# Optimization experiments

Measured on AMD Instinct MI355X. Metric: run time of the kernel, lower is better.

The kernel has to match this reference:

```python
import jax, jax.numpy as jnp
import numpy as np

N_NODES = 100000
N_EDGES = 1000000
N_GRAPHS = 2048
IN_DIM, HIDDEN, OUT_DIM = 5, 64, 128


def setup_inputs() -> dict:
    key = jax.random.key(0)
    ks = jax.random.split(key, 12)
    x = jax.random.normal(ks[0], (N_NODES, IN_DIM), dtype=jnp.float32)
    edge_index = jax.random.randint(ks[1], (2, N_EDGES), 0, N_NODES, dtype=jnp.int64)
    batch = jnp.sort(jax.random.randint(ks[2], (N_NODES,), 0, N_GRAPHS, dtype=jnp.int64))
    def lin(k, fan_in, fan_out):
        bound = 1.0 / np.sqrt(fan_in)
        kw, kb = jax.random.split(k)
        W = jax.random.uniform(kw, (fan_in, fan_out), jnp.float32, -bound, bound)
        b = jax.random.uniform(kb, (fan_out,), jnp.float32, -bound, bound)
        return W, b
    W1, b1 = lin(ks[3], IN_DIM, HIDDEN)
    W2, b2 = lin(ks[4], HIDDEN, HIDDEN)
    W3, b3 = lin(ks[5], HIDDEN, HIDDEN)
    W4, b4 = lin(ks[6], HIDDEN, OUT_DIM)
    return {"x": x, "edge_index": edge_index, "batch": batch,
            "W1": W1, "b1": b1, "W2": W2, "b2": b2,
            "W3": W3, "b3": b3, "W4": W4, "b4": b4}


def _gcn_conv(x, W, b, src, dst, norm, n):
    # h = x W; message from src, scaled by symmetric norm, scattered to dst
    h = x @ W                                   # [N, F]
    msg = h[src] * norm[:, None]                # [E+N, F] gather
    agg = jax.ops.segment_sum(msg, dst, num_segments=n)  # scatter-add
    return agg + b


def reference(x, edge_index, batch, W1, b1, W2, b2, W3, b3, W4, b4):
    n = x.shape[0]
    loop = jnp.arange(n, dtype=edge_index.dtype)
    # GCN with self-loops: src -> dst aggregation, D^-1/2 A_hat D^-1/2 norm
    src = jnp.concatenate([edge_index[0], loop])
    dst = jnp.concatenate([edge_index[1], loop])
    deg = jax.ops.segment_sum(jnp.ones_like(dst, dtype=x.dtype), dst, num_segments=n)
    dinv = jnp.where(deg > 0, jax.lax.rsqrt(jnp.maximum(deg, 1.0)), 0.0)
    norm = dinv[src] * dinv[dst]                # [E+N]

    h = jax.nn.relu(_gcn_conv(x, W1, b1, src, dst, norm, n))
    h = jax.nn.relu(_gcn_conv(h, W2, b2, src, dst, norm, n))

    # global mean pool per graph
    sums = jax.ops.segment_sum(h, batch, num_segments=N_GRAPHS)      # [G, F]
    cnts = jax.ops.segment_sum(jnp.ones((n,), h.dtype), batch, num_segments=N_GRAPHS)
    pooled = sums / jnp.maximum(cnts, 1.0)[:, None]

    # MLP head
    z = jax.nn.relu(pooled @ W3 + b3)
    return z @ W4 + b4
```

## Files before the change

### kernel.cpp

```cpp
#include <hip/hip_runtime.h>
#include <hip/hip_fp16.h>

#define N_NODES  100000
#define N_EDGES  1000000
#define N_GRAPHS 2048
#define IN_DIM   5
#define HIDDEN   64
#define OUT_DIM  128
#define CAP      32
#define NA       512
#define PART     256
#define NBIN     391
#define LSTR     72

typedef _Float16 f16x8 __attribute__((ext_vector_type(8)));
typedef float    f32x4 __attribute__((ext_vector_type(4)));

__global__ void k_hist(const int* __restrict__ dst, int* __restrict__ histT) {
    __shared__ int h[NBIN];
    int t = threadIdx.x, b = blockIdx.x;
    for (int i = t; i < NBIN; i += 256) h[i] = 0;
    __syncthreads();
    for (int e = b * 256 + t; e < N_EDGES; e += NA * 256)
        atomicAdd(&h[dst[e] >> 8], 1);
    __syncthreads();
    for (int i = t; i < NBIN; i += 256) histT[i * NA + b] = h[i];
}

__global__ void k_scanA(int* __restrict__ histT, int* __restrict__ total) {
    __shared__ int s[2][256];
    int bin = blockIdx.x, t = threadIdx.x;
    int* col = histT + bin * NA;
    int v0 = col[2 * t], v1 = col[2 * t + 1];
    int pair = v0 + v1;
    int cur = 0;
    s[0][t] = pair;
    __syncthreads();
    for (int off = 1; off < 256; off <<= 1) {
        int nv = s[cur][t] + ((t >= off) ? s[cur][t - off] : 0);
        s[cur ^ 1][t] = nv;
        cur ^= 1;
        __syncthreads();
    }
    int incl = s[cur][t];
    int excl = incl - pair;
    col[2 * t]     = excl;
    col[2 * t + 1] = excl + v0;
    if (t == 255) total[bin] = incl;
}

__global__ void k_scanB(const int* __restrict__ total, int* __restrict__ binBase) {
    __shared__ int s[2][512];
    int t = threadIdx.x;
    int v = (t < NBIN) ? total[t] : 0;
    int cur = 0;
    s[0][t] = v;
    __syncthreads();
    for (int off = 1; off < 512; off <<= 1) {
        int nv = s[cur][t] + ((t >= off) ? s[cur][t - off] : 0);
        s[cur ^ 1][t] = nv;
        cur ^= 1;
        __syncthreads();
    }
    if (t < NBIN) binBase[t] = s[cur][t] - v;
    if (t == NBIN - 1) binBase[NBIN] = s[cur][t];
}

__global__ void k_part(const int* __restrict__ src, const int* __restrict__ dst,
                       const int* __restrict__ histT, const int* __restrict__ binBase,
                       int* __restrict__ epart) {
    __shared__ int off[NBIN];
    int t = threadIdx.x, b = blockIdx.x;
    for (int i = t; i < NBIN; i += 256)
        off[i] = binBase[i] + histT[i * NA + b];
    __syncthreads();
    for (int e = b * 256 + t; e < N_EDGES; e += NA * 256) {
        int d = dst[e];
        int pos = atomicAdd(&off[d >> 8], 1);
        epart[pos] = ((d & (PART - 1)) << 17) | src[e];
    }
}

__global__ void __launch_bounds__(256) k_build(
        const int* __restrict__ epart, const int* __restrict__ binBase,
        const float* __restrict__ x, int* __restrict__ cnt, int* __restrict__ bkt,
        float* __restrict__ dinv, __half* __restrict__ xs) {
    __shared__ int lcnt[PART];
    __shared__ int lrows[PART * CAP];
    int t = threadIdx.x, b = blockIdx.x;
    int base = b * PART;
    for (int i = t; i < PART; i += 256) lcnt[i] = 0;
    __syncthreads();
    int estart = binBase[b], eend = binBase[b + 1];
    for (int i = estart + t; i < eend; i += 256) {
        int ed = epart[i];
        int ln = ed >> 17;
        int c = atomicAdd(&lcnt[ln], 1);
        if (c < CAP) lrows[ln * CAP + c] = ed & 0x1FFFF;
    }
    __syncthreads();
    int gbase = base * CAP;
    int lim = min(PART * CAP, N_NODES * CAP - gbase);
    for (int i = t; i < lim; i += 256) bkt[gbase + i] = lrows[i];
    for (int n = t; n < PART; n += 256) {
        int g = base + n;
        if (g < N_NODES) {
            int c = lcnt[n];
            cnt[g] = c;
            float d = rsqrtf(1.0f + (float)c);
            dinv[g] = d;
#pragma unroll
            for (int k = 0; k < 8; k++)
                xs[(size_t)g * 8 + k] =
                    __float2half((k < IN_DIM) ? x[g * IN_DIM + k] * d : 0.0f);
        }
    }
}

__global__ void __launch_bounds__(256) k_g5l12(
        const int* __restrict__ cnt, const int* __restrict__ bkt,
        const __half* __restrict__ xs,
        const float* __restrict__ W1, const float* __restrict__ b1,
        const float* __restrict__ W2, const float* __restrict__ dinv,
        __half* __restrict__ hs2h) {
    __shared__ _Float16 lh1[64 * LSTR];
    __shared__ _Float16 lw2[64 * LSTR];
    __shared__ float la5[64][8];
    int tid = threadIdx.x;
    int w = tid >> 6, l = tid & 63;
    int nodeBase = blockIdx.x * 64;

#pragma unroll
    for (int i = 0; i < 16; i++) {
        int idx = tid + i * 256;
        int k = idx >> 6, n = idx & 63;
        lw2[n * LSTR + k] = (_Float16)W2[k * HIDDEN + n];
    }

    {
        int g4 = l >> 2, l4 = l & 3;
        int ln = w * 16 + g4;
        int g = nodeBase + ln;
        float accx = 0.f, accy = 0.f;
        if (g < N_NODES) {
            const __half2* XH = (const __half2*)xs;
            int len = min(cnt[g], CAP);
            const int* row = bkt + (size_t)g * CAP;
            float2 self = __half22float2(XH[(size_t)g * 4 + l4]);
            accx = self.x; accy = self.y;
            for (int e = 0; e < len; e++) {
                int s = row[e];
                float2 v = __half22float2(XH[(size_t)s * 4 + l4]);
                accx += v.x; accy += v.y;
            }
            float d = dinv[g];
            accx *= d; accy *= d;
        }
        la5[ln][l4 * 2]     = accx;
        la5[ln][l4 * 2 + 1] = accy;
    }

    int f = l;
    for (int i = 0; i < 16; i++) {
        int ln = w * 16 + i;
        float t1 = b1[f];
#pragma unroll
        for (int k = 0; k < IN_DIM; k++)
            t1 += la5[ln][k] * W1[k * HIDDEN + f];
        lh1[ln * LSTR + f] = (_Float16)fmaxf(t1, 0.f);
    }
    __syncthreads();

    int quad = l >> 4, m16 = l & 15;
    f32x4 acc0 = {0.f, 0.f, 0.f, 0.f};
    f32x4 acc1 = {0.f, 0.f, 0.f, 0.f};
    f32x4 acc2 = {0.f, 0.f, 0.f, 0.f};
    f32x4 acc3 = {0.f, 0.f, 0.f, 0.f};
#pragma unroll
    for (int kc = 0; kc < 2; kc++) {
        f16x8 a = *(const f16x8*)&lh1[(w * 16 + m16) * LSTR + kc * 32 + quad * 8];
        f16x8 b0 = *(const f16x8*)&lw2[(0 * 16 + m16) * LSTR + kc * 32 + quad * 8];
        f16x8 b1f = *(const f16x8*)&lw2[(1 * 16 + m16) * LSTR + kc * 32 + quad * 8];
        f16x8 b2 = *(const f16x8*)&lw2[(2 * 16 + m16) * LSTR + kc * 32 + quad * 8];
        f16x8 b3 = *(const f16x8*)&lw2[(3 * 16 + m16) * LSTR + kc * 32 + quad * 8];
        acc0 = __builtin_amdgcn_mfma_f32_16x16x32_f16(a, b0, acc0, 0, 0, 0);
        acc1 = __builtin_amdgcn_mfma_f32_16x16x32_f16(a, b1f, acc1, 0, 0, 0);
        acc2 = __builtin_amdgcn_mfma_f32_16x16x32_f16(a, b2, acc2, 0, 0, 0);
        acc3 = __builtin_amdgcn_mfma_f32_16x16x32_f16(a, b3, acc3, 0, 0, 0);
    }
#pragma unroll
    for (int i = 0; i < 4; i++) {
        int g = nodeBase + w * 16 + quad * 4 + i;
        if (g >= N_NODES) continue;
        float dv = dinv[g];
        __half* row = hs2h + (size_t)g * HIDDEN + m16;
        row[0]  = __float2half(acc0[i] * dv);
        row[16] = __float2half(acc1[i] * dv);
        row[32] = __float2half(acc2[i] * dv);
        row[48] = __float2half(acc3[i] * dv);
    }
}

__global__ void k_gather2(const int* __restrict__ cnt, const int* __restrict__ bkt,
                          const __half* __restrict__ hs2h,
                          const float* __restrict__ dinv,
                          float* __restrict__ agg2) {
    int tid = threadIdx.x;
    int w = tid >> 6, lane = tid & 63;
    int g16 = lane >> 4, l16 = lane & 15;
    int node = blockIdx.x * 16 + w * 4 + g16;
    if (node >= N_NODES) return;
    int len = min(cnt[node], CAP);
    const int* row = bkt + (size_t)node * CAP;
    const float2* H8 = (const float2*)hs2h;
    float ax = 0.f, ay = 0.f, az = 0.f, aw = 0.f;
    float bx = 0.f, by = 0.f, bz = 0.f, bw = 0.f;
    int idx = 0;
    for (; idx + 1 < len; idx += 2) {
        int s0 = row[idx], s1 = row[idx + 1];
        float2 r0 = H8[(size_t)s0 * 16 + l16];
        float2 r1 = H8[(size_t)s1 * 16 + l16];
        const __half2* h0 = (const __half2*)&r0;
        const __half2* h1 = (const __half2*)&r1;
        float2 u0 = __half22float2(h0[0]), u1 = __half22float2(h0[1]);
        float2 v0 = __half22float2(h1[0]), v1 = __half22float2(h1[1]);
        ax += u0.x; ay += u0.y; az += u1.x; aw += u1.y;
        bx += v0.x; by += v0.y; bz += v1.x; bw += v1.y;
    }
    if (idx < len) {
        int s0 = row[idx];
        float2 r0 = H8[(size_t)s0 * 16 + l16];
        const __half2* h0 = (const __half2*)&r0;
        float2 u0 = __half22float2(h0[0]), u1 = __half22float2(h0[1]);
        ax += u0.x; ay += u0.y; az += u1.x; aw += u1.y;
    }
    float2 rs = H8[(size_t)node * 16 + l16];
    const __half2* hs = (const __half2*)&rs;
    float2 s0 = __half22float2(hs[0]), s1 = __half22float2(hs[1]);
    float d = dinv[node];
    float4 o;
    o.x = (ax + bx + s0.x) * d;
    o.y = (ay + by + s0.y) * d;
    o.z = (az + bz + s1.x) * d;
    o.w = (aw + bw + s1.y) * d;
    ((float4*)agg2)[(size_t)node * 16 + l16] = o;
}

__global__ void k_head(const float* __restrict__ agg2, const float* __restrict__ b2,
                       const int* __restrict__ batch,
                       const float* __restrict__ W3, const float* __restrict__ b3,
                       const float* __restrict__ W4, const float* __restrict__ b4,
                       float* __restrict__ out) {
    __shared__ int range[2];
    __shared__ float part[2][HIDDEN];
    __shared__ float p[HIDDEN];
    __shared__ float z[HIDDEN];
    int g = blockIdx.x, tid = threadIdx.x;
    if (tid < 2) {
        int v = g + tid;
        int lo = 0, hi = N_NODES;
        while (lo < hi) {
            int m = (lo + hi) >> 1;
            if (batch[m] < v) lo = m + 1; else hi = m;
        }
        range[tid] = lo;
    }
    __syncthreads();
    int s = range[0], e = range[1];
    int f = tid & 63, half = tid >> 6;
    float acc = 0.f;
    float bb = b2[f];
    for (int node = s + half; node < e; node += 2)
        acc += fmaxf(agg2[(size_t)node * HIDDEN + f] + bb, 0.f);
    part[half][f] = acc;
    __syncthreads();
    if (tid < HIDDEN) {
        float inv = 1.0f / fmaxf((float)(e - s), 1.0f);
        p[tid] = (part[0][tid] + part[1][tid]) * inv;
    }
    __syncthreads();
    if (tid < HIDDEN) {
        float t = b3[tid];
#pragma unroll 8
        for (int k = 0; k < HIDDEN; k++) t += p[k] * W3[k * HIDDEN + tid];
        z[tid] = fmaxf(t, 0.f);
    }
    __syncthreads();
    float t = b4[tid];
#pragma unroll 8
    for (int k = 0; k < HIDDEN; k++) t += z[k] * W4[k * OUT_DIM + tid];
    out[(size_t)g * OUT_DIM + tid] = t;
}

extern "C" void kernel_launch(void* const* d_in, const int* in_sizes, int n_in,
                              void* d_out, int out_size, void* d_ws, size_t ws_size,
                              hipStream_t stream) {
    const float* x  = (const float*)d_in[0];
    const int*   ei = (const int*)d_in[1];
    const int*   batch = (const int*)d_in[2];
    const float* W1 = (const float*)d_in[3];
    const float* b1 = (const float*)d_in[4];
    const float* W2 = (const float*)d_in[5];
    const float* b2 = (const float*)d_in[6];
    const float* W3 = (const float*)d_in[7];
    const float* b3 = (const float*)d_in[8];
    const float* W4 = (const float*)d_in[9];
    const float* b4 = (const float*)d_in[10];
    float* out = (float*)d_out;

    const int* src = ei;
    const int* dst = ei + N_EDGES;

    int*   histT   = (int*)d_ws;
    int*   total   = histT + (size_t)NBIN * NA;
    int*   binBase = total + NBIN;
    int*   cnt     = binBase + NBIN + 1;
    int*   bkt     = cnt + N_NODES;
    float* dinv    = (float*)(bkt + (size_t)N_NODES * CAP);
    __half* hs2h   = (__half*)(dinv + N_NODES);
    float* big     = (float*)(hs2h + (size_t)N_NODES * HIDDEN);
    __half* xs     = (__half*)big;
    int*   epart   = (int*)(big + (size_t)N_NODES * 16);
    float* agg2    = big;

    k_hist<<<NA, 256, 0, stream>>>(dst, histT);
    k_scanA<<<NBIN, 256, 0, stream>>>(histT, total);
    k_scanB<<<1, 512, 0, stream>>>(total, binBase);
    k_part<<<NA, 256, 0, stream>>>(src, dst, histT, binBase, epart);
    k_build<<<NBIN, 256, 0, stream>>>(epart, binBase, x, cnt, bkt, dinv, xs);

    k_g5l12<<<(N_NODES + 63) / 64, 256, 0, stream>>>(cnt, bkt, xs, W1, b1, W2,
                                                     dinv, hs2h);
    k_gather2<<<(N_NODES + 15) / 16, 256, 0, stream>>>(cnt, bkt, hs2h, dinv, agg2);

    k_head<<<N_GRAPHS, 128, 0, stream>>>(agg2, b2, batch, W3, b3, W4, b4, out);
}
```

Baseline: 193.1 us.

## Fuse layer-2 gather with mean-pool and MLP head per graph

Replaces the separate layer-2 gather kernel and the head kernel with one kernel launched per graph. Each block gathers its graph's nodes, applies bias and ReLU, and pools them in registers, then runs the MLP. This removes the fp32 agg2 write and re-read plus one launch. In exchange, parallelism drops from about 6250 blocks to 2048. Each block also copies W3 and W4 into LDS (48KB), which may lower occupancy, and the inner loop is unrolled by four.

New measurement: 216.0 us. 11.9% more time.

```diff
diff --git a/kernel.cpp b/kernel.cpp
--- a/kernel.cpp
+++ b/kernel.cpp
@@ -201,61 +201,25 @@
     }
 }
 
-__global__ void k_gather2(const int* __restrict__ cnt, const int* __restrict__ bkt,
-                          const __half* __restrict__ hs2h,
-                          const float* __restrict__ dinv,
-                          float* __restrict__ agg2) {
-    int tid = threadIdx.x;
-    int w = tid >> 6, lane = tid & 63;
-    int g16 = lane >> 4, l16 = lane & 15;
-    int node = blockIdx.x * 16 + w * 4 + g16;
-    if (node >= N_NODES) return;
-    int len = min(cnt[node], CAP);
-    const int* row = bkt + (size_t)node * CAP;
-    const float2* H8 = (const float2*)hs2h;
-    float ax = 0.f, ay = 0.f, az = 0.f, aw = 0.f;
-    float bx = 0.f, by = 0.f, bz = 0.f, bw = 0.f;
-    int idx = 0;
-    for (; idx + 1 < len; idx += 2) {
-        int s0 = row[idx], s1 = row[idx + 1];
-        float2 r0 = H8[(size_t)s0 * 16 + l16];
-        float2 r1 = H8[(size_t)s1 * 16 + l16];
-        const __half2* h0 = (const __half2*)&r0;
-        const __half2* h1 = (const __half2*)&r1;
-        float2 u0 = __half22float2(h0[0]), u1 = __half22float2(h0[1]);
-        float2 v0 = __half22float2(h1[0]), v1 = __half22float2(h1[1]);
-        ax += u0.x; ay += u0.y; az += u1.x; aw += u1.y;
-        bx += v0.x; by += v0.y; bz += v1.x; bw += v1.y;
-    }
-    if (idx < len) {
-        int s0 = row[idx];
-        float2 r0 = H8[(size_t)s0 * 16 + l16];
-        const __half2* h0 = (const __half2*)&r0;
-        float2 u0 = __half22float2(h0[0]), u1 = __half22float2(h0[1]);
-        ax += u0.x; ay += u0.y; az += u1.x; aw += u1.y;
-    }
-    float2 rs = H8[(size_t)node * 16 + l16];
-    const __half2* hs = (const __half2*)&rs;
-    float2 s0 = __half22float2(hs[0]), s1 = __half22float2(hs[1]);
-    float d = dinv[node];
-    float4 o;
-    o.x = (ax + bx + s0.x) * d;
-    o.y = (ay + by + s0.y) * d;
-    o.z = (az + bz + s1.x) * d;
-    o.w = (aw + bw + s1.y) * d;
-    ((float4*)agg2)[(size_t)node * 16 + l16] = o;
-}
-
-__global__ void k_head(const float* __restrict__ agg2, const float* __restrict__ b2,
-                       const int* __restrict__ batch,
-                       const float* __restrict__ W3, const float* __restrict__ b3,
-                       const float* __restrict__ W4, const float* __restrict__ b4,
-                       float* __restrict__ out) {
+__global__ void __launch_bounds__(256) k_g2head(
+        const int* __restrict__ cnt, const int* __restrict__ bkt,
+        const __half* __restrict__ hs2h, const float* __restrict__ dinv,
+        const int* __restrict__ batch, const float* __restrict__ b2,
+        const float* __restrict__ W3, const float* __restrict__ b3,
+        const float* __restrict__ W4, const float* __restrict__ b4,
+        float* __restrict__ out) {
+    __shared__ float w3[HIDDEN * HIDDEN];
+    __shared__ float w4[HIDDEN * OUT_DIM];
     __shared__ int range[2];
-    __shared__ float part[2][HIDDEN];
+    __shared__ float4 pool4[4][16];
     __shared__ float p[HIDDEN];
     __shared__ float z[HIDDEN];
     int g = blockIdx.x, tid = threadIdx.x;
+    int w = tid >> 6, lane = tid & 63;
+    int g16 = lane >> 4, l16 = lane & 15;
+
+    for (int i = tid; i < HIDDEN * HIDDEN; i += 256) w3[i] = W3[i];
+    for (int i = tid; i < HIDDEN * OUT_DIM; i += 256) w4[i] = W4[i];
     if (tid < 2) {
         int v = g + tid;
         int lo = 0, hi = N_NODES;
@@ -267,29 +231,86 @@
     }
     __syncthreads();
     int s = range[0], e = range[1];
-    int f = tid & 63, half = tid >> 6;
-    float acc = 0.f;
-    float bb = b2[f];
-    for (int node = s + half; node < e; node += 2)
-        acc += fmaxf(agg2[(size_t)node * HIDDEN + f] + bb, 0.f);
-    part[half][f] = acc;
-    __syncthreads();
-    if (tid < HIDDEN) {
+
+    const float2* H8 = (const float2*)hs2h;
+    float4 b2v = ((const float4*)b2)[l16];
+    float4 acc = make_float4(0.f, 0.f, 0.f, 0.f);
+    for (int node = s + w * 4 + g16; node < e; node += 16) {
+        int len = min(cnt[node], CAP);
+        const int* row = bkt + (size_t)node * CAP;
+        float ax = 0.f, ay = 0.f, az = 0.f, aw = 0.f;
+        float bxx = 0.f, bby = 0.f, bzz = 0.f, bww = 0.f;
+        float cx = 0.f, cy = 0.f, cz = 0.f, cw = 0.f;
+        float dx = 0.f, dy = 0.f, dz = 0.f, dw = 0.f;
+        int idx = 0;
+        for (; idx + 3 < len; idx += 4) {
+            int s0 = row[idx], s1 = row[idx + 1], s2 = row[idx + 2], s3 = row[idx + 3];
+            float2 r0 = H8[(size_t)s0 * 16 + l16];
+            float2 r1 = H8[(size_t)s1 * 16 + l16];
+            float2 r2 = H8[(size_t)s2 * 16 + l16];
+            float2 r3 = H8[(size_t)s3 * 16 + l16];
+            const __half2* h0 = (const __half2*)&r0;
+            const __half2* h1 = (const __half2*)&r1;
+            const __half2* h2 = (const __half2*)&r2;
+            const __half2* h3 = (const __half2*)&r3;
+            float2 u0 = __half22float2(h0[0]), u1 = __half22float2(h0[1]);
+            float2 v0 = __half22float2(h1[0]), v1 = __half22float2(h1[1]);
+            float2 q0 = __half22float2(h2[0]), q1 = __half22float2(h2[1]);
+            float2 t0 = __half22float2(h3[0]), t1 = __half22float2(h3[1]);
+            ax += u0.x; ay += u0.y; az += u1.x; aw += u1.y;
+            bxx += v0.x; bby += v0.y; bzz += v1.x; bww += v1.y;
+            cx += q0.x; cy += q0.y; cz += q1.x; cw += q1.y;
+            dx += t0.x; dy += t0.y; dz += t1.x; dw += t1.y;
+        }
+        for (; idx < len; idx++) {
+            int s0 = row[idx];
+            float2 r0 = H8[(size_t)s0 * 16 + l16];
+            const __half2* h0 = (const __half2*)&r0;
+            float2 u0 = __half22float2(h0[0]), u1 = __half22float2(h0[1]);
+            ax += u0.x; ay += u0.y; az += u1.x; aw += u1.y;
+        }
+        float2 rs = H8[(size_t)node * 16 + l16];
+        const __half2* hsp = (const __half2*)&rs;
+        float2 s0f = __half22float2(hsp[0]), s1f = __half22float2(hsp[1]);
+        float d = dinv[node];
+        float ox = (ax + bxx + cx + dx + s0f.x) * d;
+        float oy = (ay + bby + cy + dy + s0f.y) * d;
+        float oz = (az + bzz + cz + dz + s1f.x) * d;
+        float ow = (aw + bww + cw + dw + s1f.y) * d;
+        acc.x += fmaxf(ox + b2v.x, 0.f);
+        acc.y += fmaxf(oy + b2v.y, 0.f);
+        acc.z += fmaxf(oz + b2v.z, 0.f);
+        acc.w += fmaxf(ow + b2v.w, 0.f);
+    }
+    acc.x += __shfl_xor(acc.x, 16); acc.y += __shfl_xor(acc.y, 16);
+    acc.z += __shfl_xor(acc.z, 16); acc.w += __shfl_xor(acc.w, 16);
+    acc.x += __shfl_xor(acc.x, 32); acc.y += __shfl_xor(acc.y, 32);
+    acc.z += __shfl_xor(acc.z, 32); acc.w += __shfl_xor(acc.w, 32);
+    if (g16 == 0) pool4[w][l16] = acc;
+    __syncthreads();
+    if (tid < 16) {
+        float4 a0 = pool4[0][tid], a1 = pool4[1][tid];
+        float4 a2 = pool4[2][tid], a3 = pool4[3][tid];
         float inv = 1.0f / fmaxf((float)(e - s), 1.0f);
-        p[tid] = (part[0][tid] + part[1][tid]) * inv;
+        ((float4*)p)[tid] = make_float4((a0.x + a1.x + a2.x + a3.x) * inv,
+                                        (a0.y + a1.y + a2.y + a3.y) * inv,
+                                        (a0.z + a1.z + a2.z + a3.z) * inv,
+                                        (a0.w + a1.w + a2.w + a3.w) * inv);
     }
     __syncthreads();
     if (tid < HIDDEN) {
         float t = b3[tid];
 #pragma unroll 8
-        for (int k = 0; k < HIDDEN; k++) t += p[k] * W3[k * HIDDEN + tid];
+        for (int k = 0; k < HIDDEN; k++) t += p[k] * w3[k * HIDDEN + tid];
         z[tid] = fmaxf(t, 0.f);
     }
     __syncthreads();
-    float t = b4[tid];
+    if (tid < OUT_DIM) {
+        float t = b4[tid];
 #pragma unroll 8
-    for (int k = 0; k < HIDDEN; k++) t += z[k] * W4[k * OUT_DIM + tid];
-    out[(size_t)g * OUT_DIM + tid] = t;
+        for (int k = 0; k < HIDDEN; k++) t += z[k] * w4[k * OUT_DIM + tid];
+        out[(size_t)g * OUT_DIM + tid] = t;
+    }
 }
 
 extern "C" void kernel_launch(void* const* d_in, const int* in_sizes, int n_in,
@@ -321,7 +342,6 @@
     float* big     = (float*)(hs2h + (size_t)N_NODES * HIDDEN);
     __half* xs     = (__half*)big;
     int*   epart   = (int*)(big + (size_t)N_NODES * 16);
-    float* agg2    = big;
 
     k_hist<<<NA, 256, 0, stream>>>(dst, histT);
     k_scanA<<<NBIN, 256, 0, stream>>>(histT, total);
@@ -331,7 +351,6 @@
 
     k_g5l12<<<(N_NODES + 63) / 64, 256, 0, stream>>>(cnt, bkt, xs, W1, b1, W2,
                                                      dinv, hs2h);
-    k_gather2<<<(N_NODES + 15) / 16, 256, 0, stream>>>(cnt, bkt, hs2h, dinv, agg2);
-
-    k_head<<<N_GRAPHS, 128, 0, stream>>>(agg2, b2, batch, W3, b3, W4, b4, out);
-}
+    k_g2head<<<N_GRAPHS, 256, 0, stream>>>(cnt, bkt, hs2h, dinv, batch, b2,
+                                           W3, b3, W4, b4, out);
+}
```

## Fuse second-layer gather with mean-pool and MLP head per graph

Applied to the files above, without the earlier changes.

Merges the layer-2 neighbor gather kernel and the pooling/MLP head kernel into one kernel launched per graph. Each block gathers its graph's nodes with 8 lanes per node using 16-byte loads, applies bias and ReLU, and reduces into the pool directly, so the fp32 agg2 buffer is never written or read back and one launch disappears. In exchange, gather parallelism is now limited to 2048 blocks and depends on how many nodes each graph has, which may cut the latency hiding the old node-parallel gather had.

New measurement: 192.2 us. About the same (-0.5%).

```diff
diff --git a/kernel.cpp b/kernel.cpp
--- a/kernel.cpp
+++ b/kernel.cpp
@@ -201,61 +201,21 @@
     }
 }
 
-__global__ void k_gather2(const int* __restrict__ cnt, const int* __restrict__ bkt,
-                          const __half* __restrict__ hs2h,
-                          const float* __restrict__ dinv,
-                          float* __restrict__ agg2) {
-    int tid = threadIdx.x;
-    int w = tid >> 6, lane = tid & 63;
-    int g16 = lane >> 4, l16 = lane & 15;
-    int node = blockIdx.x * 16 + w * 4 + g16;
-    if (node >= N_NODES) return;
-    int len = min(cnt[node], CAP);
-    const int* row = bkt + (size_t)node * CAP;
-    const float2* H8 = (const float2*)hs2h;
-    float ax = 0.f, ay = 0.f, az = 0.f, aw = 0.f;
-    float bx = 0.f, by = 0.f, bz = 0.f, bw = 0.f;
-    int idx = 0;
-    for (; idx + 1 < len; idx += 2) {
-        int s0 = row[idx], s1 = row[idx + 1];
-        float2 r0 = H8[(size_t)s0 * 16 + l16];
-        float2 r1 = H8[(size_t)s1 * 16 + l16];
-        const __half2* h0 = (const __half2*)&r0;
-        const __half2* h1 = (const __half2*)&r1;
-        float2 u0 = __half22float2(h0[0]), u1 = __half22float2(h0[1]);
-        float2 v0 = __half22float2(h1[0]), v1 = __half22float2(h1[1]);
-        ax += u0.x; ay += u0.y; az += u1.x; aw += u1.y;
-        bx += v0.x; by += v0.y; bz += v1.x; bw += v1.y;
-    }
-    if (idx < len) {
-        int s0 = row[idx];
-        float2 r0 = H8[(size_t)s0 * 16 + l16];
-        const __half2* h0 = (const __half2*)&r0;
-        float2 u0 = __half22float2(h0[0]), u1 = __half22float2(h0[1]);
-        ax += u0.x; ay += u0.y; az += u1.x; aw += u1.y;
-    }
-    float2 rs = H8[(size_t)node * 16 + l16];
-    const __half2* hs = (const __half2*)&rs;
-    float2 s0 = __half22float2(hs[0]), s1 = __half22float2(hs[1]);
-    float d = dinv[node];
-    float4 o;
-    o.x = (ax + bx + s0.x) * d;
-    o.y = (ay + by + s0.y) * d;
-    o.z = (az + bz + s1.x) * d;
-    o.w = (aw + bw + s1.y) * d;
-    ((float4*)agg2)[(size_t)node * 16 + l16] = o;
-}
-
-__global__ void k_head(const float* __restrict__ agg2, const float* __restrict__ b2,
-                       const int* __restrict__ batch,
-                       const float* __restrict__ W3, const float* __restrict__ b3,
-                       const float* __restrict__ W4, const float* __restrict__ b4,
-                       float* __restrict__ out) {
+__global__ void __launch_bounds__(256) k_g2head(
+        const int* __restrict__ cnt, const int* __restrict__ bkt,
+        const __half* __restrict__ hs2h, const float* __restrict__ dinv,
+        const int* __restrict__ batch, const float* __restrict__ b2,
+        const float* __restrict__ W3, const float* __restrict__ b3,
+        const float* __restrict__ W4, const float* __restrict__ b4,
+        float* __restrict__ out) {
     __shared__ int range[2];
-    __shared__ float part[2][HIDDEN];
+    __shared__ float pool[4][HIDDEN];
     __shared__ float p[HIDDEN];
     __shared__ float z[HIDDEN];
     int g = blockIdx.x, tid = threadIdx.x;
+    int w = tid >> 6, lane = tid & 63;
+    int g8 = lane >> 3, l8 = lane & 7;
+
     if (tid < 2) {
         int v = g + tid;
         int lo = 0, hi = N_NODES;
@@ -267,16 +227,68 @@
     }
     __syncthreads();
     int s = range[0], e = range[1];
-    int f = tid & 63, half = tid >> 6;
-    float acc = 0.f;
-    float bb = b2[f];
-    for (int node = s + half; node < e; node += 2)
-        acc += fmaxf(agg2[(size_t)node * HIDDEN + f] + bb, 0.f);
-    part[half][f] = acc;
+
+    const float4* H16 = (const float4*)hs2h;
+    float4 b2a = ((const float4*)b2)[l8 * 2];
+    float4 b2b = ((const float4*)b2)[l8 * 2 + 1];
+    float accp[8] = {0.f, 0.f, 0.f, 0.f, 0.f, 0.f, 0.f, 0.f};
+    for (int node = s + w * 8 + g8; node < e; node += 32) {
+        int len = min(cnt[node], CAP);
+        const int* row = bkt + (size_t)node * CAP;
+        float a[8] = {0.f, 0.f, 0.f, 0.f, 0.f, 0.f, 0.f, 0.f};
+        float b[8] = {0.f, 0.f, 0.f, 0.f, 0.f, 0.f, 0.f, 0.f};
+        int idx = 0;
+        for (; idx + 1 < len; idx += 2) {
+            int s0 = row[idx], s1 = row[idx + 1];
+            float4 r0 = H16[(size_t)s0 * 8 + l8];
+            float4 r1 = H16[(size_t)s1 * 8 + l8];
+            const __half2* h0 = (const __half2*)&r0;
+            const __half2* h1 = (const __half2*)&r1;
+#pragma unroll
+            for (int k = 0; k < 4; k++) {
+                float2 u = __half22float2(h0[k]);
+                float2 v = __half22float2(h1[k]);
+                a[2 * k]     += u.x; a[2 * k + 1] += u.y;
+                b[2 * k]     += v.x; b[2 * k + 1] += v.y;
+            }
+        }
+        if (idx < len) {
+            int s0 = row[idx];
+            float4 r0 = H16[(size_t)s0 * 8 + l8];
+            const __half2* h0 = (const __half2*)&r0;
+#pragma unroll
+            for (int k = 0; k < 4; k++) {
+                float2 u = __half22float2(h0[k]);
+                a[2 * k] += u.x; a[2 * k + 1] += u.y;
+            }
+        }
+        float4 rs = H16[(size_t)node * 8 + l8];
+        const __half2* hsp = (const __half2*)&rs;
+        float d = dinv[node];
+        float bb[8] = {b2a.x, b2a.y, b2a.z, b2a.w, b2b.x, b2b.y, b2b.z, b2b.w};
+#pragma unroll
+        for (int k = 0; k < 4; k++) {
+            float2 sf = __half22float2(hsp[k]);
+            float o0 = (a[2 * k]     + b[2 * k]     + sf.x) * d;
+            float o1 = (a[2 * k + 1] + b[2 * k + 1] + sf.y) * d;
+            accp[2 * k]     += fmaxf(o0 + bb[2 * k], 0.f);
+            accp[2 * k + 1] += fmaxf(o1 + bb[2 * k + 1], 0.f);
+        }
+    }
+#pragma unroll
+    for (int k = 0; k < 8; k++) {
+        accp[k] += __shfl_xor(accp[k], 8);
+        accp[k] += __shfl_xor(accp[k], 16);
+        accp[k] += __shfl_xor(accp[k], 32);
+    }
+    if (g8 == 0) {
+#pragma unroll
+        for (int k = 0; k < 8; k++) pool[w][l8 * 8 + k] = accp[k];
+    }
     __syncthreads();
     if (tid < HIDDEN) {
         float inv = 1.0f / fmaxf((float)(e - s), 1.0f);
-        p[tid] = (part[0][tid] + part[1][tid]) * inv;
+        p[tid] = (pool[0][tid] + pool[1][tid] + pool[2][tid] + pool[3][tid]) * inv;
     }
     __syncthreads();
     if (tid < HIDDEN) {
@@ -286,10 +298,12 @@
         z[tid] = fmaxf(t, 0.f);
     }
     __syncthreads();
-    float t = b4[tid];
+    if (tid < OUT_DIM) {
+        float t = b4[tid];
 #pragma unroll 8
-    for (int k = 0; k < HIDDEN; k++) t += z[k] * W4[k * OUT_DIM + tid];
-    out[(size_t)g * OUT_DIM + tid] = t;
+        for (int k = 0; k < HIDDEN; k++) t += z[k] * W4[k * OUT_DIM + tid];
+        out[(size_t)g * OUT_DIM + tid] = t;
+    }
 }
 
 extern "C" void kernel_launch(void* const* d_in, const int* in_sizes, int n_in,
@@ -321,7 +335,6 @@
     float* big     = (float*)(hs2h + (size_t)N_NODES * HIDDEN);
     __half* xs     = (__half*)big;
     int*   epart   = (int*)(big + (size_t)N_NODES * 16);
-    float* agg2    = big;
 
     k_hist<<<NA, 256, 0, stream>>>(dst, histT);
     k_scanA<<<NBIN, 256, 0, stream>>>(histT, total);
@@ -331,7 +344,6 @@
 
     k_g5l12<<<(N_NODES + 63) / 64, 256, 0, stream>>>(cnt, bkt, xs, W1, b1, W2,
                                                      dinv, hs2h);
-    k_gather2<<<(N_NODES + 15) / 16, 256, 0, stream>>>(cnt, bkt, hs2h, dinv, agg2);
-
-    k_head<<<N_GRAPHS, 128, 0, stream>>>(agg2, b2, batch, W3, b3, W4, b4, out);
-}
+    k_g2head<<<N_GRAPHS, 256, 0, stream>>>(cnt, bkt, hs2h, dinv, batch, b2,
+                                           W3, b3, W4, b4, out);
+}
```
